# Performance work log

Hardware: AMD Instinct MI355X
Metric: run time of the kernel (lower is better)

Reference implementation:

```python
import jax, jax.numpy as jnp
import numpy as np

EPS = 1e-5

def layernorm(x, gamma, beta):
    mu = jnp.mean(x, axis=-1, keepdims=True)
    var = jnp.mean(jnp.square(x - mu), axis=-1, keepdims=True)
    return (x - mu) * jax.lax.rsqrt(var + EPS) * gamma + beta

def setup_inputs() -> dict:
    key = jax.random.key(0)
    ks = jax.random.split(key, 5)
    B, I, H = 8192, 1024, 1024
    x = jax.random.normal(ks[0], (B, I), dtype=jnp.float32)
    hx = jax.random.normal(ks[1], (B, H), dtype=jnp.float32)
    cx = jax.random.normal(ks[2], (B, H), dtype=jnp.float32)
    W_ih = jax.random.normal(ks[3], (4 * H, I), dtype=jnp.float32)
    W_hh = jax.random.normal(ks[4], (4 * H, H), dtype=jnp.float32)
    gamma_i = jnp.ones((4 * H,), jnp.float32); beta_i = jnp.zeros((4 * H,), jnp.float32)
    gamma_h = jnp.ones((4 * H,), jnp.float32); beta_h = jnp.zeros((4 * H,), jnp.float32)
    gamma_c = jnp.ones((H,), jnp.float32); beta_c = jnp.zeros((H,), jnp.float32)
    return {"x": x, "hx": hx, "cx": cx, "W_ih": W_ih, "W_hh": W_hh,
            "gamma_i": gamma_i, "beta_i": beta_i,
            "gamma_h": gamma_h, "beta_h": beta_h,
            "gamma_c": gamma_c, "beta_c": beta_c}

def reference(x, hx, cx, W_ih, W_hh, gamma_i, beta_i, gamma_h, beta_h, gamma_c, beta_c):
    # igates/hgates: [B, 4H]
    igates = layernorm(x @ W_ih.T, gamma_i, beta_i)
    hgates = layernorm(hx @ W_hh.T, gamma_h, beta_h)
    gates = igates + hgates
    i, f, g, o = jnp.split(gates, 4, axis=1)
    i = jax.nn.sigmoid(i)
    f = jax.nn.sigmoid(f)
    g = jnp.tanh(g)
    o = jax.nn.sigmoid(o)
    cy = layernorm(f * cx + i * g, gamma_c, beta_c)
    hy = o * jnp.tanh(cy)
    return (hy, (hy, cy))
```

## Files before the change

kernel.cpp:

```cpp
#include <hip/hip_runtime.h>

typedef __attribute__((ext_vector_type(8))) short short8_t;
typedef __attribute__((ext_vector_type(4))) float f32x4;

#define AS1 __attribute__((address_space(1)))
#define AS3 __attribute__((address_space(3)))

__device__ inline void gload_lds16(const void* g, void* l) {
  __builtin_amdgcn_global_load_lds((AS1 void*)g, (AS3 void*)l, 16, 0, 0);
}

__device__ inline unsigned short f2bf(float f) {
  unsigned int u = __builtin_bit_cast(unsigned int, f);
  u += 0x7fffu + ((u >> 16) & 1u);
  return (unsigned short)(u >> 16);
}
__device__ inline float bfu2f(unsigned short u) {
  return __builtin_bit_cast(float, ((unsigned int)u) << 16);
}
__device__ inline float sigmoidf_(float x) {
  x = fminf(fmaxf(x, -30.f), 30.f);
  return 1.f / (1.f + __expf(-x));
}
__device__ inline float tanhf_(float x) {
  x = fminf(fmaxf(x, -15.f), 15.f);
  float e = __expf(2.f * x);
  return (e - 1.f) / (e + 1.f);
}

__global__ __launch_bounds__(256) void cvt_bf16(const float* __restrict__ src,
                                                unsigned short* __restrict__ dst,
                                                int n) {
  int i = (blockIdx.x * 256 + threadIdx.x) * 8;
  if (i >= n) return;
  const float4* s = reinterpret_cast<const float4*>(src + i);
  float4 a = s[0], b = s[1];
  union { unsigned short us[8]; uint4 v; } o;
  o.us[0] = f2bf(a.x); o.us[1] = f2bf(a.y); o.us[2] = f2bf(a.z); o.us[3] = f2bf(a.w);
  o.us[4] = f2bf(b.x); o.us[5] = f2bf(b.y); o.us[6] = f2bf(b.z); o.us[7] = f2bf(b.w);
  *reinterpret_cast<uint4*>(dst + i) = o.v;
}

__global__ __launch_bounds__(512, 2) void gemm_dual(
    const unsigned short* __restrict__ Xb, const unsigned short* __restrict__ Hxb,
    const unsigned short* __restrict__ Wib, const unsigned short* __restrict__ Whb,
    unsigned short* __restrict__ Gi, unsigned short* __restrict__ Gh) {
  const int K = 1024, N = 4096;
  const unsigned short* A  = blockIdx.z ? Hxb : Xb;
  const unsigned short* Bw = blockIdx.z ? Whb : Wib;
  unsigned short* C        = blockIdx.z ? Gh : Gi;

  __shared__ __align__(16) unsigned short lA[3 * 256 * 32];
  __shared__ __align__(16) unsigned short lB[3 * 256 * 32];

  const int t    = threadIdx.x;
  const int wid  = t >> 6;
  const int lane = t & 63;
  const int fr = lane & 15, fq = lane >> 4;
  const int m0 = blockIdx.y * 256, n0 = blockIdx.x * 256;
  const int wrb = (wid >> 1) * 64;
  const int wcb = (wid & 1) * 128;

  auto stage = [&](int kt, int sbuf) {
    const int k0 = kt * 32;
#pragma unroll
    for (int g = 0; g < 2; ++g) {
      int idx = g * 512 + t;
      int row = idx >> 2;
      int ls  = (idx & 3) ^ ((idx >> 3) & 3);
      const unsigned short* ga = A  + (size_t)(m0 + row) * K + k0 + ls * 8;
      const unsigned short* gb = Bw + (size_t)(n0 + row) * K + k0 + ls * 8;
      unsigned short* la = lA + sbuf * 8192 + g * 4096 + wid * 512;
      unsigned short* lb = lB + sbuf * 8192 + g * 4096 + wid * 512;
      gload_lds16(ga, la);
      gload_lds16(gb, lb);
    }
  };

  f32x4 acc[4][8];
#pragma unroll
  for (int i = 0; i < 4; ++i)
#pragma unroll
    for (int j = 0; j < 8; ++j) acc[i][j] = (f32x4){0.f, 0.f, 0.f, 0.f};

  stage(0, 0);
  stage(1, 1);
  asm volatile("s_waitcnt vmcnt(4)" ::: "memory");
  __builtin_amdgcn_sched_barrier(0);
  __builtin_amdgcn_s_barrier();
  __builtin_amdgcn_sched_barrier(0);

  const int NT = K / 32;
  const int swz = (fq ^ ((fr >> 1) & 3)) * 8;

  int cur = 0;
  for (int kt = 0; kt < NT; ++kt) {
    if (kt + 2 < NT) {
      int n2 = cur + 2; if (n2 >= 3) n2 -= 3;
      stage(kt + 2, n2);
    }
    const unsigned short* a_base = lA + cur * 8192;
    const unsigned short* b_base = lB + cur * 8192;

    short8_t bv[8], av[4];
#pragma unroll
    for (int j = 0; j < 8; ++j)
      bv[j] = *reinterpret_cast<const short8_t*>(b_base + (wcb + j * 16 + fr) * 32 + swz);
#pragma unroll
    for (int i = 0; i < 4; ++i)
      av[i] = *reinterpret_cast<const short8_t*>(a_base + (wrb + i * 16 + fr) * 32 + swz);

    __builtin_amdgcn_s_setprio(1);
#pragma unroll
    for (int i = 0; i < 4; ++i)
#pragma unroll
      for (int j = 0; j < 8; ++j)
        acc[i][j] = __builtin_amdgcn_mfma_f32_16x16x32_bf16(av[i], bv[j], acc[i][j], 0, 0, 0);
    __builtin_amdgcn_s_setprio(0);

    if (kt < NT - 1) {
      if (kt + 2 < NT) {
        asm volatile("s_waitcnt vmcnt(4)" ::: "memory");
      } else {
        asm volatile("s_waitcnt vmcnt(0)" ::: "memory");
      }
      __builtin_amdgcn_sched_barrier(0);
      __builtin_amdgcn_s_barrier();
      __builtin_amdgcn_sched_barrier(0);
    }
    cur = (cur + 1 == 3) ? 0 : cur + 1;
  }

#pragma unroll
  for (int i = 0; i < 4; ++i)
#pragma unroll
    for (int j = 0; j < 8; ++j)
#pragma unroll
      for (int r = 0; r < 4; ++r) {
        int row = m0 + wrb + i * 16 + fq * 4 + r;
        int col = n0 + wcb + j * 16 + fr;
        C[(size_t)row * N + col] = f2bf(acc[i][j][r]);
      }
}

__global__ __launch_bounds__(256) void fuse_ln_lstm(
    const unsigned short* __restrict__ Gi, const unsigned short* __restrict__ Gh,
    const float* __restrict__ cx,
    const float* __restrict__ gi_g, const float* __restrict__ gi_b,
    const float* __restrict__ gh_g, const float* __restrict__ gh_b,
    const float* __restrict__ gc_g, const float* __restrict__ gc_b,
    float* __restrict__ out) {
  const int H = 1024;
  const size_t BH = (size_t)8192 * 1024;
  const int b = blockIdx.x, t = threadIdx.x;
  const int wid = t >> 6, lane = t & 63;

  __shared__ __align__(16) unsigned short lgi[4096];
  __shared__ __align__(16) unsigned short lgh[4096];
  __shared__ float lred[32];

  const uint4* gi_row = reinterpret_cast<const uint4*>(Gi) + (size_t)b * 512;
  const uint4* gh_row = reinterpret_cast<const uint4*>(Gh) + (size_t)b * 512;

  float si = 0.f, qi = 0.f, sh = 0.f, qh = 0.f;
#pragma unroll
  for (int c = 0; c < 2; ++c) {
    uint4 v = gi_row[c * 256 + t];
    uint4 w = gh_row[c * 256 + t];
    *reinterpret_cast<uint4*>(&lgi[(c * 256 + t) * 8]) = v;
    *reinterpret_cast<uint4*>(&lgh[(c * 256 + t) * 8]) = w;
    unsigned int uv[4] = {v.x, v.y, v.z, v.w};
    unsigned int uw[4] = {w.x, w.y, w.z, w.w};
#pragma unroll
    for (int e = 0; e < 4; ++e) {
      float a0 = __builtin_bit_cast(float, uv[e] << 16);
      float a1 = __builtin_bit_cast(float, uv[e] & 0xffff0000u);
      si += a0 + a1; qi += a0 * a0 + a1 * a1;
      float b0 = __builtin_bit_cast(float, uw[e] << 16);
      float b1 = __builtin_bit_cast(float, uw[e] & 0xffff0000u);
      sh += b0 + b1; qh += b0 * b0 + b1 * b1;
    }
  }
#pragma unroll
  for (int s = 32; s; s >>= 1) {
    si += __shfl_xor(si, s); qi += __shfl_xor(qi, s);
    sh += __shfl_xor(sh, s); qh += __shfl_xor(qh, s);
  }
  if (lane == 0) { lred[wid] = si; lred[4 + wid] = qi; lred[8 + wid] = sh; lred[12 + wid] = qh; }
  __syncthreads();
  float Si = lred[0] + lred[1] + lred[2] + lred[3];
  float Qi = lred[4] + lred[5] + lred[6] + lred[7];
  float Sh = lred[8] + lred[9] + lred[10] + lred[11];
  float Qh = lred[12] + lred[13] + lred[14] + lred[15];
  const float inv4096 = 1.f / 4096.f;
  float mui = Si * inv4096;
  float rsi = rsqrtf(fmaxf(Qi * inv4096 - mui * mui, 0.f) + 1e-5f);
  float muh = Sh * inv4096;
  float rsh = rsqrtf(fmaxf(Qh * inv4096 - muh * muh, 0.f) + 1e-5f);

  float cv[4], ov[4];
  float sc = 0.f, qc = 0.f;
#pragma unroll
  for (int k = 0; k < 4; ++k) {
    int h = t + 256 * k;
    float g0 = bfu2f(lgi[h]),        h0 = bfu2f(lgh[h]);
    float g1 = bfu2f(lgi[h + 1024]), h1 = bfu2f(lgh[h + 1024]);
    float g2 = bfu2f(lgi[h + 2048]), h2 = bfu2f(lgh[h + 2048]);
    float g3 = bfu2f(lgi[h + 3072]), h3 = bfu2f(lgh[h + 3072]);
    float vi = (g0 - mui) * rsi * gi_g[h]        + gi_b[h]        + (h0 - muh) * rsh * gh_g[h]        + gh_b[h];
    float vf = (g1 - mui) * rsi * gi_g[h + 1024] + gi_b[h + 1024] + (h1 - muh) * rsh * gh_g[h + 1024] + gh_b[h + 1024];
    float vg = (g2 - mui) * rsi * gi_g[h + 2048] + gi_b[h + 2048] + (h2 - muh) * rsh * gh_g[h + 2048] + gh_b[h + 2048];
    float vo = (g3 - mui) * rsi * gi_g[h + 3072] + gi_b[h + 3072] + (h3 - muh) * rsh * gh_g[h + 3072] + gh_b[h + 3072];
    float ig = sigmoidf_(vi), fg = sigmoidf_(vf), gg = tanhf_(vg), og = sigmoidf_(vo);
    float c = fg * cx[(size_t)b * H + h] + ig * gg;
    cv[k] = c; ov[k] = og;
    sc += c; qc += c * c;
  }
#pragma unroll
  for (int s = 32; s; s >>= 1) { sc += __shfl_xor(sc, s); qc += __shfl_xor(qc, s); }
  if (lane == 0) { lred[16 + wid] = sc; lred[20 + wid] = qc; }
  __syncthreads();
  float Sc = lred[16] + lred[17] + lred[18] + lred[19];
  float Qc = lred[20] + lred[21] + lred[22] + lred[23];
  const float inv1024 = 1.f / 1024.f;
  float muc = Sc * inv1024;
  float rsc = rsqrtf(fmaxf(Qc * inv1024 - muc * muc, 0.f) + 1e-5f);
#pragma unroll
  for (int k = 0; k < 4; ++k) {
    int h = t + 256 * k;
    float cy = (cv[k] - muc) * rsc * gc_g[h] + gc_b[h];
    float hy = ov[k] * tanhf_(cy);
    size_t o0 = (size_t)b * H + h;
    out[o0] = hy;
    out[BH + o0] = hy;
    out[2 * BH + o0] = cy;
  }
}

extern "C" void kernel_launch(void* const* d_in, const int* in_sizes, int n_in,
                              void* d_out, int out_size, void* d_ws, size_t ws_size,
                              hipStream_t stream) {
  const float* x    = (const float*)d_in[0];
  const float* hx   = (const float*)d_in[1];
  const float* cx   = (const float*)d_in[2];
  const float* Wih  = (const float*)d_in[3];
  const float* Whh  = (const float*)d_in[4];
  const float* gi_g = (const float*)d_in[5];
  const float* gi_b = (const float*)d_in[6];
  const float* gh_g = (const float*)d_in[7];
  const float* gh_b = (const float*)d_in[8];
  const float* gc_g = (const float*)d_in[9];
  const float* gc_b = (const float*)d_in[10];
  float* out = (float*)d_out;

  const size_t NB = (size_t)8192 * 1024;
  const size_t NW = (size_t)4096 * 1024;
  const size_t NG = (size_t)8192 * 4096;

  unsigned short* ws  = (unsigned short*)d_ws;
  unsigned short* xb  = ws;
  unsigned short* hxb = xb + NB;
  unsigned short* wib = hxb + NB;
  unsigned short* whb = wib + NW;
  unsigned short* Gi  = whb + NW;
  unsigned short* Gh  = Gi + NG;

  cvt_bf16<<<(int)(NB / 2048), 256, 0, stream>>>(x, xb, (int)NB);
  cvt_bf16<<<(int)(NB / 2048), 256, 0, stream>>>(hx, hxb, (int)NB);
  cvt_bf16<<<(int)(NW / 2048), 256, 0, stream>>>(Wih, wib, (int)NW);
  cvt_bf16<<<(int)(NW / 2048), 256, 0, stream>>>(Whh, whb, (int)NW);

  dim3 gg(4096 / 256, 8192 / 256, 2);
  gemm_dual<<<gg, 512, 0, stream>>>(xb, hxb, wib, whb, Gi, Gh);

  fuse_ln_lstm<<<8192, 256, 0, stream>>>(Gi, Gh, cx, gi_g, gi_b, gh_g, gh_b,
                                         gc_g, gc_b, out);
}
```

Baseline: 275.6 us.

## Restructure bf16 GEMM into 8-wave ping-pong schedule with 64-wide K tiles

Rewrites the dual GEMM main loop to use 64-wide K tiles with double buffering instead of 32-wide triple buffering. The warp layout changes to 2x4 waves, each covering a 128x64 sub-tile. Each K step is split into four MFMA phases, with the LDS fragment reads and global-to-LDS staging interleaved between barriers. The aim is to overlap memory traffic with MFMA work and cut LDS read volume per MFMA. In exchange it adds many more barriers per iteration, and the subtler vmcnt accounting risks stalls or correctness issues.

```diff
diff --git a/kernel.cpp b/kernel.cpp
--- a/kernel.cpp
+++ b/kernel.cpp
@@ -45,101 +45,167 @@
     const unsigned short* __restrict__ Xb, const unsigned short* __restrict__ Hxb,
     const unsigned short* __restrict__ Wib, const unsigned short* __restrict__ Whb,
     unsigned short* __restrict__ Gi, unsigned short* __restrict__ Gh) {
-  const int K = 1024, N = 4096;
+  const int K = 1024, N = 4096, NT = 16;
   const unsigned short* A  = blockIdx.z ? Hxb : Xb;
   const unsigned short* Bw = blockIdx.z ? Whb : Wib;
   unsigned short* C        = blockIdx.z ? Gh : Gi;
 
-  __shared__ __align__(16) unsigned short lA[3 * 256 * 32];
-  __shared__ __align__(16) unsigned short lB[3 * 256 * 32];
+  __shared__ __align__(16) unsigned short lA[2 * 2 * 128 * 64];
+  __shared__ __align__(16) unsigned short lB[2 * 2 * 128 * 64];
 
   const int t    = threadIdx.x;
   const int wid  = t >> 6;
   const int lane = t & 63;
   const int fr = lane & 15, fq = lane >> 4;
+  const int wm = wid >> 2;
+  const int wn = wid & 3;
   const int m0 = blockIdx.y * 256, n0 = blockIdx.x * 256;
-  const int wrb = (wid >> 1) * 64;
-  const int wcb = (wid & 1) * 128;
-
-  auto stage = [&](int kt, int sbuf) {
-    const int k0 = kt * 32;
+
+  auto stage = [&](int kt, int X, int h) {
+    if (kt >= NT) return;
+    const unsigned short* G = X ? Bw : A;
+    const int r0 = (X ? n0 : m0) + h * 128;
+    unsigned short* L = (X ? lB : lA) + (kt & 1) * 16384 + h * 8192;
 #pragma unroll
     for (int g = 0; g < 2; ++g) {
       int idx = g * 512 + t;
-      int row = idx >> 2;
-      int ls  = (idx & 3) ^ ((idx >> 3) & 3);
-      const unsigned short* ga = A  + (size_t)(m0 + row) * K + k0 + ls * 8;
-      const unsigned short* gb = Bw + (size_t)(n0 + row) * K + k0 + ls * 8;
-      unsigned short* la = lA + sbuf * 8192 + g * 4096 + wid * 512;
-      unsigned short* lb = lB + sbuf * 8192 + g * 4096 + wid * 512;
-      gload_lds16(ga, la);
-      gload_lds16(gb, lb);
+      int row = idx >> 3;
+      int ls  = (idx & 7) ^ (row & 7);
+      gload_lds16(G + (size_t)(r0 + row) * K + kt * 64 + ls * 8,
+                  L + g * 4096 + wid * 512);
     }
   };
 
-  f32x4 acc[4][8];
-#pragma unroll
-  for (int i = 0; i < 4; ++i)
-#pragma unroll
-    for (int j = 0; j < 8; ++j) acc[i][j] = (f32x4){0.f, 0.f, 0.f, 0.f};
-
-  stage(0, 0);
-  stage(1, 1);
+  f32x4 acc[8][4];
+#pragma unroll
+  for (int i = 0; i < 8; ++i)
+#pragma unroll
+    for (int j = 0; j < 4; ++j) acc[i][j] = (f32x4){0.f, 0.f, 0.f, 0.f};
+
+  stage(0, 0, 0); stage(0, 0, 1); stage(0, 1, 0); stage(0, 1, 1);
+  stage(1, 0, 0); stage(1, 0, 1);
   asm volatile("s_waitcnt vmcnt(4)" ::: "memory");
   __builtin_amdgcn_sched_barrier(0);
   __builtin_amdgcn_s_barrier();
   __builtin_amdgcn_sched_barrier(0);
 
-  const int NT = K / 32;
-  const int swz = (fq ^ ((fr >> 1) & 3)) * 8;
-
-  int cur = 0;
+  const int sw0 = ((fq)     ^ (fr & 7)) * 8;
+  const int sw1 = ((fq + 4) ^ (fr & 7)) * 8;
+  const int bro = (wn & 1) * 64;
+
+  short8_t av[4][2], bv[4][2];
+
   for (int kt = 0; kt < NT; ++kt) {
+    const unsigned short* As = lA + (kt & 1) * 16384 + wm * 8192;
+    const unsigned short* Bs = lB + (kt & 1) * 16384 + (wn >> 1) * 8192;
+
+#pragma unroll
+    for (int m = 0; m < 4; ++m) {
+      av[m][0] = *reinterpret_cast<const short8_t*>(As + (m * 16 + fr) * 64 + sw0);
+      av[m][1] = *reinterpret_cast<const short8_t*>(As + (m * 16 + fr) * 64 + sw1);
+    }
+#pragma unroll
+    for (int n = 0; n < 2; ++n) {
+      bv[n][0] = *reinterpret_cast<const short8_t*>(Bs + (bro + n * 16 + fr) * 64 + sw0);
+      bv[n][1] = *reinterpret_cast<const short8_t*>(Bs + (bro + n * 16 + fr) * 64 + sw1);
+    }
+    stage(kt + 1, 1, 0);
+    __builtin_amdgcn_sched_barrier(0);
+    __builtin_amdgcn_s_barrier();
+    asm volatile("s_waitcnt lgkmcnt(0)" ::: "memory");
+    __builtin_amdgcn_sched_barrier(0);
+    __builtin_amdgcn_s_setprio(1);
+#pragma unroll
+    for (int m = 0; m < 4; ++m)
+#pragma unroll
+      for (int n = 0; n < 2; ++n)
+#pragma unroll
+        for (int ks = 0; ks < 2; ++ks)
+          acc[m][n] = __builtin_amdgcn_mfma_f32_16x16x32_bf16(av[m][ks], bv[n][ks], acc[m][n], 0, 0, 0);
+    __builtin_amdgcn_s_setprio(0);
+    __builtin_amdgcn_sched_barrier(0);
+    __builtin_amdgcn_s_barrier();
+    __builtin_amdgcn_sched_barrier(0);
+
+#pragma unroll
+    for (int n = 2; n < 4; ++n) {
+      bv[n][0] = *reinterpret_cast<const short8_t*>(Bs + (bro + n * 16 + fr) * 64 + sw0);
+      bv[n][1] = *reinterpret_cast<const short8_t*>(Bs + (bro + n * 16 + fr) * 64 + sw1);
+    }
+    stage(kt + 1, 1, 1);
+    __builtin_amdgcn_sched_barrier(0);
+    __builtin_amdgcn_s_barrier();
+    asm volatile("s_waitcnt lgkmcnt(0)" ::: "memory");
+    __builtin_amdgcn_sched_barrier(0);
+    __builtin_amdgcn_s_setprio(1);
+#pragma unroll
+    for (int m = 0; m < 4; ++m)
+#pragma unroll
+      for (int n = 2; n < 4; ++n)
+#pragma unroll
+        for (int ks = 0; ks < 2; ++ks)
+          acc[m][n] = __builtin_amdgcn_mfma_f32_16x16x32_bf16(av[m][ks], bv[n][ks], acc[m][n], 0, 0, 0);
+    __builtin_amdgcn_s_setprio(0);
+    __builtin_amdgcn_sched_barrier(0);
+    __builtin_amdgcn_s_barrier();
+    __builtin_amdgcn_sched_barrier(0);
+
+#pragma unroll
+    for (int m = 0; m < 4; ++m) {
+      av[m][0] = *reinterpret_cast<const short8_t*>(As + ((m + 4) * 16 + fr) * 64 + sw0);
+      av[m][1] = *reinterpret_cast<const short8_t*>(As + ((m + 4) * 16 + fr) * 64 + sw1);
+    }
+    __builtin_amdgcn_sched_barrier(0);
+    __builtin_amdgcn_s_barrier();
+    asm volatile("s_waitcnt lgkmcnt(0)" ::: "memory");
+    __builtin_amdgcn_sched_barrier(0);
+    __builtin_amdgcn_s_setprio(1);
+#pragma unroll
+    for (int m = 0; m < 4; ++m)
+#pragma unroll
+      for (int n = 0; n < 2; ++n)
+#pragma unroll
+        for (int ks = 0; ks < 2; ++ks)
+          acc[m + 4][n] = __builtin_amdgcn_mfma_f32_16x16x32_bf16(av[m][ks], bv[n][ks], acc[m + 4][n], 0, 0, 0);
+    __builtin_amdgcn_s_setprio(0);
+    __builtin_amdgcn_sched_barrier(0);
+    __builtin_amdgcn_s_barrier();
+    __builtin_amdgcn_sched_barrier(0);
+
+    stage(kt + 2, 0, 0);
+    stage(kt + 2, 0, 1);
+    __builtin_amdgcn_sched_barrier(0);
+    __builtin_amdgcn_s_barrier();
+    asm volatile("s_waitcnt lgkmcnt(0)" ::: "memory");
+    __builtin_amdgcn_sched_barrier(0);
+    __builtin_amdgcn_s_setprio(1);
+#pragma unroll
+    for (int m = 0; m < 4; ++m)
+#pragma unroll
+      for (int n = 2; n < 4; ++n)
+#pragma unroll
+        for (int ks = 0; ks < 2; ++ks)
+          acc[m + 4][n] = __builtin_amdgcn_mfma_f32_16x16x32_bf16(av[m][ks], bv[n][ks], acc[m + 4][n], 0, 0, 0);
+    __builtin_amdgcn_s_setprio(0);
     if (kt + 2 < NT) {
-      int n2 = cur + 2; if (n2 >= 3) n2 -= 3;
-      stage(kt + 2, n2);
-    }
-    const unsigned short* a_base = lA + cur * 8192;
-    const unsigned short* b_base = lB + cur * 8192;
-
-    short8_t bv[8], av[4];
-#pragma unroll
-    for (int j = 0; j < 8; ++j)
-      bv[j] = *reinterpret_cast<const short8_t*>(b_base + (wcb + j * 16 + fr) * 32 + swz);
-#pragma unroll
-    for (int i = 0; i < 4; ++i)
-      av[i] = *reinterpret_cast<const short8_t*>(a_base + (wrb + i * 16 + fr) * 32 + swz);
-
-    __builtin_amdgcn_s_setprio(1);
-#pragma unroll
-    for (int i = 0; i < 4; ++i)
-#pragma unroll
-      for (int j = 0; j < 8; ++j)
-        acc[i][j] = __builtin_amdgcn_mfma_f32_16x16x32_bf16(av[i], bv[j], acc[i][j], 0, 0, 0);
-    __builtin_amdgcn_s_setprio(0);
-
-    if (kt < NT - 1) {
-      if (kt + 2 < NT) {
-        asm volatile("s_waitcnt vmcnt(4)" ::: "memory");
-      } else {
-        asm volatile("s_waitcnt vmcnt(0)" ::: "memory");
-      }
-      __builtin_amdgcn_sched_barrier(0);
-      __builtin_amdgcn_s_barrier();
-      __builtin_amdgcn_sched_barrier(0);
-    }
-    cur = (cur + 1 == 3) ? 0 : cur + 1;
-  }
-
-#pragma unroll
-  for (int i = 0; i < 4; ++i)
-#pragma unroll
-    for (int j = 0; j < 8; ++j)
+      asm volatile("s_waitcnt vmcnt(4)" ::: "memory");
+    } else if (kt + 1 < NT) {
+      asm volatile("s_waitcnt vmcnt(0)" ::: "memory");
+    }
+    __builtin_amdgcn_sched_barrier(0);
+    __builtin_amdgcn_s_barrier();
+    __builtin_amdgcn_sched_barrier(0);
+  }
+
+#pragma unroll
+  for (int m = 0; m < 8; ++m)
+#pragma unroll
+    for (int n = 0; n < 4; ++n)
 #pragma unroll
       for (int r = 0; r < 4; ++r) {
-        int row = m0 + wrb + i * 16 + fq * 4 + r;
-        int col = n0 + wcb + j * 16 + fr;
-        C[(size_t)row * N + col] = f2bf(acc[i][j][r]);
+        int row = m0 + wm * 128 + m * 16 + fq * 4 + r;
+        int col = n0 + wn * 64 + n * 16 + fr;
+        C[(size_t)row * N + col] = f2bf(acc[m][n][r]);
       }
 }
 
```

Result: faster. 246.2 us (-10.7%).

## Merge bf16 conversions into one launch and reshape GEMM warp tiling

Applied to the files above, without the earlier changes.

Replaces the four separate fp32-to-bf16 conversion launches with a single kernel that picks its source and destination from the block index, removing three launch overheads. The GEMM changes its warp layout from 4x2 (64x128 per warp) to 2x4 (128x64 per warp), so each warp loads 8 A fragments and 4 B fragments per k-step. The loop also drops the sched_barriers, adds an explicit lgkmcnt wait before the MFMAs, and now runs a barrier on every iteration, including the last. The new layout changes the LDS read pattern and register use, and removing the scheduling fences can let the compiler reorder instructions differently.

```diff
diff --git a/kernel.cpp b/kernel.cpp
--- a/kernel.cpp
+++ b/kernel.cpp
@@ -28,11 +28,18 @@
   return (e - 1.f) / (e + 1.f);
 }
 
-__global__ __launch_bounds__(256) void cvt_bf16(const float* __restrict__ src,
-                                                unsigned short* __restrict__ dst,
-                                                int n) {
-  int i = (blockIdx.x * 256 + threadIdx.x) * 8;
-  if (i >= n) return;
+__global__ __launch_bounds__(256) void cvt_bf16_all(
+    const float* __restrict__ x,  unsigned short* __restrict__ xb,
+    const float* __restrict__ hx, unsigned short* __restrict__ hxb,
+    const float* __restrict__ Wi, unsigned short* __restrict__ wib,
+    const float* __restrict__ Wh, unsigned short* __restrict__ whb) {
+  int blk = blockIdx.x;
+  const float* src; unsigned short* dst;
+  if (blk < 4096)       { src = x;  dst = xb; }
+  else if (blk < 8192)  { src = hx; dst = hxb; blk -= 4096; }
+  else if (blk < 10240) { src = Wi; dst = wib; blk -= 8192; }
+  else                  { src = Wh; dst = whb; blk -= 10240; }
+  int i = (blk * 256 + threadIdx.x) * 8;
   const float4* s = reinterpret_cast<const float4*>(src + i);
   float4 a = s[0], b = s[1];
   union { unsigned short us[8]; uint4 v; } o;
@@ -45,7 +52,7 @@
     const unsigned short* __restrict__ Xb, const unsigned short* __restrict__ Hxb,
     const unsigned short* __restrict__ Wib, const unsigned short* __restrict__ Whb,
     unsigned short* __restrict__ Gi, unsigned short* __restrict__ Gh) {
-  const int K = 1024, N = 4096;
+  const int K = 1024, N = 4096, NT = 32;
   const unsigned short* A  = blockIdx.z ? Hxb : Xb;
   const unsigned short* Bw = blockIdx.z ? Whb : Wib;
   unsigned short* C        = blockIdx.z ? Gh : Gi;
@@ -57,89 +64,81 @@
   const int wid  = t >> 6;
   const int lane = t & 63;
   const int fr = lane & 15, fq = lane >> 4;
+  const int wm = wid >> 2;
+  const int wn = wid & 3;
   const int m0 = blockIdx.y * 256, n0 = blockIdx.x * 256;
-  const int wrb = (wid >> 1) * 64;
-  const int wcb = (wid & 1) * 128;
-
-  auto stage = [&](int kt, int sbuf) {
+
+  auto stage = [&](int kt, int sb) {
+    if (kt >= NT) return;
     const int k0 = kt * 32;
 #pragma unroll
     for (int g = 0; g < 2; ++g) {
       int idx = g * 512 + t;
       int row = idx >> 2;
       int ls  = (idx & 3) ^ ((idx >> 3) & 3);
-      const unsigned short* ga = A  + (size_t)(m0 + row) * K + k0 + ls * 8;
-      const unsigned short* gb = Bw + (size_t)(n0 + row) * K + k0 + ls * 8;
-      unsigned short* la = lA + sbuf * 8192 + g * 4096 + wid * 512;
-      unsigned short* lb = lB + sbuf * 8192 + g * 4096 + wid * 512;
-      gload_lds16(ga, la);
-      gload_lds16(gb, lb);
+      gload_lds16(A  + (size_t)(m0 + row) * K + k0 + ls * 8,
+                  lA + sb * 8192 + g * 4096 + wid * 512);
+      gload_lds16(Bw + (size_t)(n0 + row) * K + k0 + ls * 8,
+                  lB + sb * 8192 + g * 4096 + wid * 512);
     }
   };
 
-  f32x4 acc[4][8];
-#pragma unroll
-  for (int i = 0; i < 4; ++i)
-#pragma unroll
-    for (int j = 0; j < 8; ++j) acc[i][j] = (f32x4){0.f, 0.f, 0.f, 0.f};
+  f32x4 acc[8][4];
+#pragma unroll
+  for (int i = 0; i < 8; ++i)
+#pragma unroll
+    for (int j = 0; j < 4; ++j) acc[i][j] = (f32x4){0.f, 0.f, 0.f, 0.f};
 
   stage(0, 0);
   stage(1, 1);
-  asm volatile("s_waitcnt vmcnt(4)" ::: "memory");
-  __builtin_amdgcn_sched_barrier(0);
+  asm volatile("s_waitcnt vmcnt(4)");
   __builtin_amdgcn_s_barrier();
-  __builtin_amdgcn_sched_barrier(0);
-
-  const int NT = K / 32;
+
   const int swz = (fq ^ ((fr >> 1) & 3)) * 8;
 
-  int cur = 0;
+  short8_t av[8], bv[4];
+
+  int rb = 0;
   for (int kt = 0; kt < NT; ++kt) {
+    int sb = rb + 2; if (sb >= 3) sb -= 3;
+    stage(kt + 2, sb);
+
+    const unsigned short* As = lA + rb * 8192;
+    const unsigned short* Bs = lB + rb * 8192;
+#pragma unroll
+    for (int m = 0; m < 8; ++m)
+      av[m] = *reinterpret_cast<const short8_t*>(As + (wm * 128 + m * 16 + fr) * 32 + swz);
+#pragma unroll
+    for (int n = 0; n < 4; ++n)
+      bv[n] = *reinterpret_cast<const short8_t*>(Bs + (wn * 64 + n * 16 + fr) * 32 + swz);
+
+    asm volatile("s_waitcnt lgkmcnt(0)");
+    __builtin_amdgcn_s_setprio(1);
+#pragma unroll
+    for (int m = 0; m < 8; ++m)
+#pragma unroll
+      for (int n = 0; n < 4; ++n)
+        acc[m][n] = __builtin_amdgcn_mfma_f32_16x16x32_bf16(av[m], bv[n], acc[m][n], 0, 0, 0);
+    __builtin_amdgcn_s_setprio(0);
+
     if (kt + 2 < NT) {
-      int n2 = cur + 2; if (n2 >= 3) n2 -= 3;
-      stage(kt + 2, n2);
+      asm volatile("s_waitcnt vmcnt(4)");
+    } else if (kt + 1 < NT) {
+      asm volatile("s_waitcnt vmcnt(0)");
     }
-    const unsigned short* a_base = lA + cur * 8192;
-    const unsigned short* b_base = lB + cur * 8192;
-
-    short8_t bv[8], av[4];
-#pragma unroll
-    for (int j = 0; j < 8; ++j)
-      bv[j] = *reinterpret_cast<const short8_t*>(b_base + (wcb + j * 16 + fr) * 32 + swz);
-#pragma unroll
-    for (int i = 0; i < 4; ++i)
-      av[i] = *reinterpret_cast<const short8_t*>(a_base + (wrb + i * 16 + fr) * 32 + swz);
-
-    __builtin_amdgcn_s_setprio(1);
-#pragma unroll
-    for (int i = 0; i < 4; ++i)
-#pragma unroll
-      for (int j = 0; j < 8; ++j)
-        acc[i][j] = __builtin_amdgcn_mfma_f32_16x16x32_bf16(av[i], bv[j], acc[i][j], 0, 0, 0);
-    __builtin_amdgcn_s_setprio(0);
-
-    if (kt < NT - 1) {
-      if (kt + 2 < NT) {
-        asm volatile("s_waitcnt vmcnt(4)" ::: "memory");
-      } else {
-        asm volatile("s_waitcnt vmcnt(0)" ::: "memory");
-      }
-      __builtin_amdgcn_sched_barrier(0);
-      __builtin_amdgcn_s_barrier();
-      __builtin_amdgcn_sched_barrier(0);
-    }
-    cur = (cur + 1 == 3) ? 0 : cur + 1;
-  }
-
-#pragma unroll
-  for (int i = 0; i < 4; ++i)
-#pragma unroll
-    for (int j = 0; j < 8; ++j)
+    __builtin_amdgcn_s_barrier();
+    rb = (rb + 1 == 3) ? 0 : rb + 1;
+  }
+
+#pragma unroll
+  for (int m = 0; m < 8; ++m)
+#pragma unroll
+    for (int n = 0; n < 4; ++n)
 #pragma unroll
       for (int r = 0; r < 4; ++r) {
-        int row = m0 + wrb + i * 16 + fq * 4 + r;
-        int col = n0 + wcb + j * 16 + fr;
-        C[(size_t)row * N + col] = f2bf(acc[i][j][r]);
+        int row = m0 + wm * 128 + m * 16 + fq * 4 + r;
+        int col = n0 + wn * 64 + n * 16 + fr;
+        C[(size_t)row * N + col] = f2bf(acc[m][n][r]);
       }
 }
 
@@ -265,10 +264,7 @@
   unsigned short* Gi  = whb + NW;
   unsigned short* Gh  = Gi + NG;
 
-  cvt_bf16<<<(int)(NB / 2048), 256, 0, stream>>>(x, xb, (int)NB);
-  cvt_bf16<<<(int)(NB / 2048), 256, 0, stream>>>(hx, hxb, (int)NB);
-  cvt_bf16<<<(int)(NW / 2048), 256, 0, stream>>>(Wih, wib, (int)NW);
-  cvt_bf16<<<(int)(NW / 2048), 256, 0, stream>>>(Whh, whb, (int)NW);
+  cvt_bf16_all<<<12288, 256, 0, stream>>>(x, xb, hx, hxb, Wih, wib, Whh, whb);
 
   dim3 gg(4096 / 256, 8192 / 256, 2);
   gemm_dual<<<gg, 512, 0, stream>>>(xb, hxb, wib, whb, Gi, Gh);
```

After: 264.6 us. -4.0%, faster.
